# Kernel optimization log

Measured on AMD Instinct MI355X. Metric: run time of the kernel, lower is better.

Reference implementation:

```python
import jax, jax.numpy as jnp
import numpy as np
import math

N_FFT = 1024
HOP = 256
N_FRAMES = 16384
SR = 24000
FFT_BIN = N_FFT // 2 + 1
EPS = 1e-11


def hann(n):
    # torch.hann_window default (periodic=True)
    return 0.5 * (1.0 - jnp.cos(2.0 * jnp.pi * jnp.arange(n, dtype=jnp.float32) / n))


def linear_interp(x, scale):
    # x: [B, T] -> [B, T*scale]; matches F.interpolate(mode='linear', align_corners=False)
    T = x.shape[-1]
    pos = (jnp.arange(T * scale, dtype=jnp.float32) + 0.5) / scale - 0.5
    pos = jnp.clip(pos, 0.0, T - 1.0)
    lo = jnp.floor(pos).astype(jnp.int32)
    hi = jnp.minimum(lo + 1, T - 1)
    frac = pos - lo.astype(jnp.float32)
    return x[:, lo] * (1.0 - frac) + x[:, hi] * frac


def impulse_train(f0, hop_length, sample_rate):
    # f0: [B, n_frames] -> impulse train [B, n_frames*hop]
    f0_up = linear_interp(f0, hop_length)
    phase = jnp.cumsum(f0_up, axis=-1) / sample_rate
    saw = jnp.mod(phase, 1.0)
    imp = saw - jnp.roll(saw, -1, axis=-1) + f0_up / sample_rate
    # original runs under torch.no_grad()
    return jax.lax.stop_gradient(imp)


def stft(x, n_fft, hop, window):
    # torch.stft(center=True, pad_mode='reflect', onesided, normalized=False)
    pad = n_fft // 2
    xp = jnp.pad(x, ((0, 0), (pad, pad)), mode="reflect")
    nf = (xp.shape[-1] - n_fft) // hop + 1
    idx = jnp.arange(nf)[:, None] * hop + jnp.arange(n_fft)[None, :]
    frames = xp[:, idx] * window  # [B, nf, n_fft]
    return jnp.fft.rfft(frames, axis=-1).transpose(0, 2, 1)  # [B, bins, nf]


def istft(S, n_fft, hop, window):
    # torch.istft(center=True): windowed overlap-add, divide by sum of squared windows
    B = S.shape[0]
    frames = jnp.fft.irfft(S.transpose(0, 2, 1), n=n_fft, axis=-1) * window  # [B, nf, n_fft]
    nf = frames.shape[1]
    out_len = n_fft + (nf - 1) * hop
    idx = jnp.arange(nf)[:, None] * hop + jnp.arange(n_fft)[None, :]
    sig = jnp.zeros((B, out_len), frames.dtype).at[:, idx].add(frames)
    wsq = jnp.zeros((out_len,), frames.dtype).at[idx].add(
        jnp.broadcast_to(window * window, (nf, n_fft))
    )
    pad = n_fft // 2
    return sig[:, pad:-pad] / jnp.maximum(wsq[pad:-pad], EPS)


def spectral_envelope_filter(signal, envelope, n_fft, hop):
    w = hann(n_fft)
    S = stft(signal, n_fft, hop, w)[:, :, 1:]  # drop first frame -> [B, bins, n_frames]
    return istft(S * envelope, n_fft, hop, w)


def estimate_minimum_phase(amp):
    # amp: [B, bins, T] real positive envelope; cepstral min-phase along dim 1
    n = (amp.shape[1] - 1) * 2
    cep = jnp.fft.irfft(jnp.log(amp), n=n, axis=1)
    fold = jnp.concatenate(
        [jnp.ones((1,), jnp.float32),
         2.0 * jnp.ones((n // 2 - 1,), jnp.float32),
         jnp.ones((1,), jnp.float32),
         jnp.zeros((n // 2 - 1,), jnp.float32)]
    )
    cep = cep * fold[None, :, None]
    return jnp.exp(jnp.fft.rfft(cep, axis=1))  # complex min-phase spectrum [B, bins, T]


def setup_inputs() -> dict:
    key = jax.random.key(0)
    k1, k2, k3 = jax.random.split(key, 3)
    log_f0 = jnp.full((1, N_FRAMES), math.log(100.0), dtype=jnp.float32)
    spec_env_noi = jax.random.normal(k1, (1, FFT_BIN, N_FRAMES), jnp.float32) - 6.0
    spec_env_per = jax.random.normal(k2, (1, FFT_BIN, N_FRAMES), jnp.float32) - 6.0
    noise = jax.random.normal(k3, (1, HOP * N_FRAMES), jnp.float32)
    return {"log_f0": log_f0, "spec_env_noi": spec_env_noi,
            "spec_env_per": spec_env_per, "noise": noise}


def reference(log_f0, spec_env_noi, spec_env_per, noise):
    pulse = impulse_train(jnp.exp(log_f0), HOP, SR)
    noi = spectral_envelope_filter(noise, jnp.exp(spec_env_noi), N_FFT, HOP)
    per = spectral_envelope_filter(
        pulse, estimate_minimum_phase(jnp.exp(spec_env_per)), N_FFT, HOP
    )
    return noi + per  # [1, (N_FRAMES-1)*HOP]
```

## Files before the change

kernel.cpp:

```cpp
#include <hip/hip_runtime.h>
#include <math.h>

#define L_TOT 4194304
#define NFR   16384
#define OUTN  4194048


__device__ __forceinline__ int lvl_off(int a) {
  return L_TOT - (L_TOT >> (a - 1));
}

__device__ __forceinline__ int swz(int e) {
  return e ^ (((e >> 4) & 3) * 5);
}

__device__ __forceinline__ float f0_up_val(const float* f0arr, int j) {
  float pos = __fadd_rn(__fmul_rn(__fadd_rn((float)j, 0.5f), 1.0f / 256.0f), -0.5f);
  pos = fminf(fmaxf(pos, 0.0f), 16383.0f);
  int lo = (int)pos;
  int hi = min(lo + 1, NFR - 1);
  float frac = __fadd_rn(pos, -(float)lo);
  float a = __fmul_rn(f0arr[lo], __fadd_rn(1.0f, -frac));
  float b = __fmul_rn(f0arr[hi], frac);
  return __fadd_rn(a, b);
}

__device__ float prefix_sum(const float* W, const float* f0arr, int m) {
  float acc = 0.0f;
  bool first = true;
  int pos = 0;
  for (int a = 22; a >= 1; --a) {
    if (m & (1 << a)) {
      float node = W[lvl_off(a) + (pos >> a)];
      acc = first ? node : __fadd_rn(acc, node);
      first = false;
      pos += (1 << a);
    }
  }
  if (m & 1) {
    float node = f0_up_val(f0arr, pos);
    acc = first ? node : __fadd_rn(acc, node);
  }
  return acc;
}

__global__ __launch_bounds__(256) void init_tables(const float* __restrict__ logf0,
                                                   float* __restrict__ W) {
  int g = blockIdx.x * 256 + threadIdx.x;
  float* twc = W + 2 * L_TOT;
  float* tws = twc + 512;
  float* wh  = twc + 1024;
  float* f0arr = twc + 2048;
  if (g < 512) {
    double a = (double)g * 3.14159265358979323846 / 512.0;
    twc[g] = (float)cos(a);
    tws[g] = (float)sin(a);
  }
  if (g < 1024) {
    double a = (double)g * 3.14159265358979323846 / 512.0;
    wh[g] = (float)(0.5 - 0.5 * cos(a));
  }
  if (g >= 2048 && g < 2048 + NFR) {
    f0arr[g - 2048] = (float)exp((double)logf0[g - 2048]);
  }
}

__global__ __launch_bounds__(256) void tree_kernel(float* W) {
  const float* f0arr = W + 2 * L_TOT + 2048;
  __shared__ float A[2048];
  __shared__ float B[1024];
  int tid = threadIdx.x;
  int base = blockIdx.x * 2048;
  for (int i = tid; i < 2048; i += 256) A[i] = f0_up_val(f0arr, base + i);
  __syncthreads();
  float* src = A;
  float* dst = B;
  int cnt = 1024;
  for (int a = 1; a <= 11; ++a) {
    int gbase = base >> a;
    for (int i = tid; i < cnt; i += 256) {
      float v = __fadd_rn(src[2 * i], src[2 * i + 1]);
      dst[i] = v;
      if (a == 11) W[lvl_off(11) + gbase + i] = v;
    }
    __syncthreads();
    float* tmp = src; src = dst; dst = tmp;
    cnt >>= 1;
  }
}

__global__ __launch_bounds__(256) void tree_top_kernel(float* W) {
  __shared__ float A[2048];
  __shared__ float B[1024];
  int tid = threadIdx.x;
  for (int i = tid; i < 2048; i += 256) A[i] = W[lvl_off(11) + i];
  __syncthreads();
  float* src = A;
  float* dst = B;
  int cnt = 1024;
  for (int a = 12; a <= 22; ++a) {
    for (int i = tid; i < cnt; i += 256) {
      float v = __fadd_rn(src[2 * i], src[2 * i + 1]);
      dst[i] = v;
      W[lvl_off(a) + i] = v;
    }
    __syncthreads();
    float* tmp = src; src = dst; dst = tmp;
    cnt >>= 1;
  }
}

__global__ __launch_bounds__(256) void pulse_kernel(float* W) {
  const float* f0arr = W + 2 * L_TOT + 2048;
  __shared__ float Tl[510];
  __shared__ float P[4100];
  int tid = threadIdx.x;
  int base = blockIdx.x * 4096;

  float v[16];
#pragma unroll
  for (int c = 0; c < 16; ++c) v[c] = f0_up_val(f0arr, base + 16 * tid + c);
  float s2[8], s4[4], s8[2];
#pragma unroll
  for (int j = 0; j < 8; ++j) s2[j] = __fadd_rn(v[2 * j], v[2 * j + 1]);
#pragma unroll
  for (int j = 0; j < 4; ++j) s4[j] = __fadd_rn(s2[2 * j], s2[2 * j + 1]);
  s8[0] = __fadd_rn(s4[0], s4[1]);
  s8[1] = __fadd_rn(s4[2], s4[3]);
  Tl[tid] = __fadd_rn(s8[0], s8[1]);
  __syncthreads();
  if (tid < 128) Tl[256 + tid] = __fadd_rn(Tl[2 * tid], Tl[2 * tid + 1]);
  __syncthreads();
  if (tid < 64)  Tl[384 + tid] = __fadd_rn(Tl[256 + 2 * tid], Tl[256 + 2 * tid + 1]);
  __syncthreads();
  if (tid < 32)  Tl[448 + tid] = __fadd_rn(Tl[384 + 2 * tid], Tl[384 + 2 * tid + 1]);
  __syncthreads();
  if (tid < 16)  Tl[480 + tid] = __fadd_rn(Tl[448 + 2 * tid], Tl[448 + 2 * tid + 1]);
  __syncthreads();
  if (tid < 8)   Tl[496 + tid] = __fadd_rn(Tl[480 + 2 * tid], Tl[480 + 2 * tid + 1]);
  __syncthreads();
  if (tid < 4)   Tl[504 + tid] = __fadd_rn(Tl[496 + 2 * tid], Tl[496 + 2 * tid + 1]);
  __syncthreads();
  if (tid < 2)   Tl[508 + tid] = __fadd_rn(Tl[504 + 2 * tid], Tl[504 + 2 * tid + 1]);
  __syncthreads();

  float accT = 0.0f;
  bool firstT = true;
  {
    int pos = 0;
    for (int a = 22; a >= 12; --a) {
      if (base & (1 << a)) {
        float node = W[lvl_off(a) + (pos >> a)];
        accT = firstT ? node : __fadd_rn(accT, node);
        firstT = false;
        pos += (1 << a);
      }
    }
  }
  float accM = accT;
  bool firstM = firstT;
  {
    int rh = 16 * tid;
    int lpos = 0;
    for (int a = 11; a >= 4; --a) {
      if (rh & (1 << a)) {
        float node = Tl[512 - (512 >> (a - 4)) + (lpos >> a)];
        accM = firstM ? node : __fadd_rn(accM, node);
        firstM = false;
        lpos += (1 << a);
      }
    }
  }
  if (tid >= 1) P[16 * tid] = accM;
#pragma unroll
  for (int c = 1; c <= 15; ++c) {
    float acc = accM;
    bool first = firstM;
    int lp = 0;
    if (c & 8) { float n = s8[lp >> 3]; acc = first ? n : __fadd_rn(acc, n); first = false; lp += 8; }
    if (c & 4) { float n = s4[lp >> 2]; acc = first ? n : __fadd_rn(acc, n); first = false; lp += 4; }
    if (c & 2) { float n = s2[lp >> 1]; acc = first ? n : __fadd_rn(acc, n); first = false; lp += 2; }
    if (c & 1) { float n = v[lp];       acc = first ? n : __fadd_rn(acc, n); }
    P[16 * tid + c] = acc;
  }
  if (tid == 0) P[4096] = prefix_sum(W, f0arr, base + 4096);
  if (tid == 1) {
    int m2 = base + 4097;
    P[4097] = (m2 <= L_TOT) ? prefix_sum(W, f0arr, m2) : 0.0f;
  }
  __syncthreads();

  float o[16];
#pragma unroll
  for (int c = 0; c < 16; ++c) {
    int i = base + 16 * tid + c;
    float P1 = P[16 * tid + c + 1];
    float P2 = (i == L_TOT - 1) ? prefix_sum(W, f0arr, 1)
                                : P[16 * tid + c + 2];
    float t1 = __fdiv_rn(P1, 24000.0f);
    float saw1 = __fadd_rn(t1, -floorf(t1));
    float t2 = __fdiv_rn(P2, 24000.0f);
    float saw2 = __fadd_rn(t2, -floorf(t2));
    float cc = __fdiv_rn(v[c], 24000.0f);
    o[c] = __fadd_rn(__fadd_rn(saw1, -saw2), cc);
  }
#pragma unroll
  for (int k = 0; k < 4; ++k)
    *(float4*)&W[L_TOT + base + 16 * tid + 4 * k] =
        make_float4(o[4 * k], o[4 * k + 1], o[4 * k + 2], o[4 * k + 3]);
}

template <int DIR>
__device__ void fft1024_r4(float2* X, float2* Pb, const float2* tw) {
  int tid = threadIdx.x;
  float2* S = X;
  float2* D = Pb;
  __syncthreads();
#pragma unroll
  for (int s = 0; s < 5; ++s) {
    int m = 1 << (2 * s);
    int b = tid;
    int t = b & ~(m - 1);
    float2 twu = tw[t];
    float ur = twu.x, ui = (DIR > 0) ? twu.y : -twu.y;
    float vr = ur * ur - ui * ui;
    float vi = 2.0f * ur * ui;
    float w3r = ur * vr - ui * vi;
    float w3i = ur * vi + ui * vr;
    float2 x0 = S[swz(b)], x1 = S[swz(b + 256)], x2 = S[swz(b + 512)], x3 = S[swz(b + 768)];
    float s0r = x0.x + x2.x, s0i = x0.y + x2.y;
    float s1r = x1.x + x3.x, s1i = x1.y + x3.y;
    float d0r = x0.x - x2.x, d0i = x0.y - x2.y;
    float e1r = x1.x - x3.x, e1i = x1.y - x3.y;
    float ser = (DIR > 0) ? -e1i : e1i;
    float sei = (DIR > 0) ? e1r : -e1r;
    int d0 = b + 3 * t;
    D[swz(d0)] = make_float2(s0r + s1r, s0i + s1i);
    float t1r = d0r + ser, t1i = d0i + sei;
    D[swz(d0 + m)] = make_float2(t1r * ur - t1i * ui, t1r * ui + t1i * ur);
    float t2r = s0r - s1r, t2i = s0i - s1i;
    D[swz(d0 + 2 * m)] = make_float2(t2r * vr - t2i * vi, t2r * vi + t2i * vr);
    float t3r = d0r - ser, t3i = d0i - sei;
    D[swz(d0 + 3 * m)] = make_float2(t3r * w3r - t3i * w3i, t3r * w3i + t3i * w3r);
    __syncthreads();
    float2* tmp = S; S = D; D = tmp;
  }
}

__device__ __forceinline__ float hann_w(int i, const float2* tw) {
  int j = (i > 512) ? (1024 - i) : i;
  float c = (j <= 256) ? tw[j].x : -tw[512 - j].x;
  return 0.5f - 0.5f * c;
}

__device__ __forceinline__ void combine_one(int k, float An, const float2* Y, float2* H) {
  int k2 = (1024 - k) & 1023;
  float2 z = Y[swz(k)], mm = Y[swz(k2)];
  float Ar = 0.5f * (z.x + mm.x), Ai = 0.5f * (z.y - mm.y);
  float Br = 0.5f * (z.y + mm.y), Bi = 0.5f * (mm.x - z.x);
  float2 h = H[k];
  H[k] = make_float2(Br * h.x - Bi * h.y + Ar * An,
                     Br * h.y + Bi * h.x + Ai * An);
}

__global__ __launch_bounds__(256) void column_kernel(
    const float* __restrict__ noise,
    const float* __restrict__ envn,
    const float* __restrict__ envp,
    const float* __restrict__ W,
    float* __restrict__ out) {
  __shared__ float2 F[1024], Y[1024];
  __shared__ float2 hA[513], hB[513];
  __shared__ float2 tw[257];
  int tid = threadIdx.x;
  int bid = blockIdx.x;
  int g = (bid & 7) * 1024 + (bid >> 3);
  int fA = 2 * g;
  const float* pulse = W + L_TOT;
  const float* gtab = W + 2 * L_TOT;

  for (int i = tid; i < 257; i += 256) tw[i] = make_float2(gtab[i], gtab[512 + i]);
  for (int k = tid; k < 513; k += 256) {
    float2 e = *(const float2*)&envp[k * NFR + fA];
    hA[k] = e;
  }
  __syncthreads();

  for (int i = tid; i < 1024; i += 256) {
    int k = (i <= 512) ? i : 1024 - i;
    F[swz(i)] = hA[k];
  }
  fft1024_r4<+1>(F, Y, tw);
  {
    float2 a0 = Y[swz(tid)], a1 = Y[swz(tid + 256)], a2 = Y[swz(tid + 512)];
    float s0 = (tid == 0) ? (1.0f / 1024.0f) : (2.0f / 1024.0f);
    F[swz(tid)] = make_float2(a0.x * s0, a0.y * s0);
    F[swz(tid + 256)] = make_float2(a1.x * (2.0f / 1024.0f), a1.y * (2.0f / 1024.0f));
    F[swz(tid + 512)] = (tid == 0) ? make_float2(a2.x * (1.0f / 1024.0f),
                                                 a2.y * (1.0f / 1024.0f))
                                   : make_float2(0.0f, 0.0f);
    F[swz(tid + 768)] = make_float2(0.0f, 0.0f);
  }
  fft1024_r4<-1>(F, Y, tw);
  for (int k = tid; k < 513; k += 256) {
    int k2 = (1024 - k) & 1023;
    float2 z = Y[swz(k)], mm = Y[swz(k2)];
    float GAr = 0.5f * (z.x + mm.x), GAi = 0.5f * (z.y - mm.y);
    float GBr = 0.5f * (z.y + mm.y), GBi = 0.5f * (mm.x - z.x);
    float er = expf(GAr);
    float si, co;
    sincosf(GAi, &si, &co);
    hA[k] = make_float2(er * co, er * si);
    er = expf(GBr);
    sincosf(GBi, &si, &co);
    hB[k] = make_float2(er * co, er * si);
  }

  for (int i = tid; i < 1024; i += 256) {
    int q = 256 * fA - 256 + i;
    if (q < 0) q = -q;
    else if (q >= L_TOT) q = 2 * L_TOT - 2 - q;
    float wv = hann_w(i, tw);
    F[swz(i)] = make_float2(noise[q] * wv, pulse[q] * wv);
  }
  fft1024_r4<-1>(F, Y, tw);
  float2 eA0 = *(const float2*)&envn[tid * NFR + fA];
  combine_one(tid, expf(eA0.x), Y, hA);
  float2 eA1 = *(const float2*)&envn[(tid + 256) * NFR + fA];
  combine_one(tid + 256, expf(eA1.x), Y, hA);
  float2 eA2 = make_float2(0.0f, 0.0f);
  if (tid == 0) {
    eA2 = *(const float2*)&envn[512 * NFR + fA];
    combine_one(512, expf(eA2.x), Y, hA);
  }

  for (int i = tid; i < 1024; i += 256) {
    int q = 256 * fA + i;
    if (q >= L_TOT) q = 2 * L_TOT - 2 - q;
    float wv = hann_w(i, tw);
    F[swz(i)] = make_float2(noise[q] * wv, pulse[q] * wv);
  }
  fft1024_r4<-1>(F, Y, tw);
  combine_one(tid, expf(eA0.y), Y, hB);
  combine_one(tid + 256, expf(eA1.y), Y, hB);
  if (tid == 0) combine_one(512, expf(eA2.y), Y, hB);
  __syncthreads();

  for (int i = tid; i < 1024; i += 256) {
    if (i <= 512) {
      F[swz(i)] = make_float2(hA[i].x - hB[i].y, hA[i].y + hB[i].x);
    } else {
      int j = 1024 - i;
      F[swz(i)] = make_float2(hA[j].x + hB[j].y, hB[j].x - hA[j].y);
    }
  }
  fft1024_r4<+1>(F, Y, tw);
  const float sc = 1.0f / 1536.0f;
  for (int i = tid; i < 1280; i += 256) {
    float val = 0.0f;
    if (i < 1024) val = Y[swz(i)].x * (hann_w(i, tw) * sc);
    if (i >= 256) {
      int j = i - 256;
      val += Y[swz(j)].y * (hann_w(j, tw) * sc);
    }
    int t = 256 * fA - 512 + i;
    if (t >= 0 && t < OUTN) atomicAdd(&out[t], val);
  }
}

__global__ __launch_bounds__(256) void finalize_kernel(float* __restrict__ out,
                                                       const float* __restrict__ W) {
  const float* wh = W + 2 * L_TOT + 1024;
  int tid = threadIdx.x;
  int t = (blockIdx.x == 0) ? tid : (OUTN - 256 + tid);
  int p = t + 512;
  int jmin = max(0, (p - 768) >> 8);
  int jmax = min(NFR - 1, p >> 8);
  float wsq = 0.0f;
  for (int j = jmin; j <= jmax; ++j) {
    float w = wh[p - 256 * j];
    wsq += w * w;
  }
  out[t] = out[t] * (1.5f / fmaxf(wsq, 1e-11f));
}

extern "C" void kernel_launch(void* const* d_in, const int* in_sizes, int n_in,
                              void* d_out, int out_size, void* d_ws, size_t ws_size,
                              hipStream_t stream) {
  const float* logf0 = (const float*)d_in[0];
  const float* envn  = (const float*)d_in[1];
  const float* envp  = (const float*)d_in[2];
  const float* noise = (const float*)d_in[3];
  float* out = (float*)d_out;
  float* W = (float*)d_ws;

  init_tables<<<dim3(72), dim3(256), 0, stream>>>(logf0, W);
  tree_kernel<<<dim3(2048), dim3(256), 0, stream>>>(W);
  tree_top_kernel<<<dim3(1), dim3(256), 0, stream>>>(W);
  pulse_kernel<<<dim3(L_TOT / 4096), dim3(256), 0, stream>>>(W);
  hipMemsetAsync(d_out, 0, (size_t)out_size * sizeof(float), stream);
  column_kernel<<<dim3(NFR / 2), dim3(256), 0, stream>>>(noise, envn, envp, W, out);
  finalize_kernel<<<dim3(2), dim3(256), 0, stream>>>(out, W);
}
```

Measured before the change: 244.5 us.

## Use in-place DIF/DIT FFTs with digit-reversed ordering and register twiddles

Replaces the ping-pong Stockham radix-4 FFT with in-place DIF and DIT variants that share one LDS buffer, pairing them so the digit-reversed order between them cancels and spectral indexing goes through dr4. Twiddles and Hann window values are preloaded into registers instead of an LDS table, and the swizzle gains more XOR terms to reduce bank conflicts for the new access strides. Halving LDS use and adding launch_bounds(256,8) targets higher occupancy, at the cost of extra syncs and a more complex index mapping.

Result: slower. 675.8 us (+176.4%).

```diff
diff --git a/kernel.cpp b/kernel.cpp
--- a/kernel.cpp
+++ b/kernel.cpp
@@ -11,7 +11,13 @@
 }
 
 __device__ __forceinline__ int swz(int e) {
-  return e ^ (((e >> 4) & 3) * 5);
+  int h = (e >> 4) & 3, g = (e >> 6) & 3, f = (e >> 8) & 3;
+  return e ^ (h * 5) ^ (g * 3) ^ ((f * 12) & 15);
+}
+
+__device__ __forceinline__ int dr4(int p) {
+  return ((p & 3) << 8) | (((p >> 2) & 3) << 6) | (((p >> 4) & 3) << 4) |
+         (((p >> 6) & 3) << 2) | ((p >> 8) & 3);
 }
 
 __device__ __forceinline__ float f0_up_val(const float* f0arr, int j) {
@@ -211,51 +217,74 @@
 }
 
 template <int DIR>
-__device__ void fft1024_r4(float2* X, float2* Pb, const float2* tw) {
-  int tid = threadIdx.x;
-  float2* S = X;
-  float2* D = Pb;
+__device__ __forceinline__ void fft_dif(float2* F, const float2 (&twr)[4]) {
+  int tid = threadIdx.x;
   __syncthreads();
 #pragma unroll
   for (int s = 0; s < 5; ++s) {
-    int m = 1 << (2 * s);
-    int b = tid;
-    int t = b & ~(m - 1);
-    float2 twu = tw[t];
-    float ur = twu.x, ui = (DIR > 0) ? twu.y : -twu.y;
-    float vr = ur * ur - ui * ui;
-    float vi = 2.0f * ur * ui;
-    float w3r = ur * vr - ui * vi;
-    float w3i = ur * vi + ui * vr;
-    float2 x0 = S[swz(b)], x1 = S[swz(b + 256)], x2 = S[swz(b + 512)], x3 = S[swz(b + 768)];
+    int L = 256 >> (2 * s);
+    int q = tid & (L - 1);
+    int base = ((tid >> (8 - 2 * s)) << (10 - 2 * s)) | q;
+    float ur, ui;
+    if (s < 4) { ur = twr[s].x; ui = twr[s].y; } else { ur = 1.0f; ui = 0.0f; }
+    if (DIR < 0) ui = -ui;
+    int e0 = swz(base), e1 = swz(base + L), e2 = swz(base + 2 * L), e3 = swz(base + 3 * L);
+    float2 x0 = F[e0], x1 = F[e1], x2 = F[e2], x3 = F[e3];
     float s0r = x0.x + x2.x, s0i = x0.y + x2.y;
     float s1r = x1.x + x3.x, s1i = x1.y + x3.y;
     float d0r = x0.x - x2.x, d0i = x0.y - x2.y;
-    float e1r = x1.x - x3.x, e1i = x1.y - x3.y;
-    float ser = (DIR > 0) ? -e1i : e1i;
-    float sei = (DIR > 0) ? e1r : -e1r;
-    int d0 = b + 3 * t;
-    D[swz(d0)] = make_float2(s0r + s1r, s0i + s1i);
-    float t1r = d0r + ser, t1i = d0i + sei;
-    D[swz(d0 + m)] = make_float2(t1r * ur - t1i * ui, t1r * ui + t1i * ur);
-    float t2r = s0r - s1r, t2i = s0i - s1i;
-    D[swz(d0 + 2 * m)] = make_float2(t2r * vr - t2i * vi, t2r * vi + t2i * vr);
-    float t3r = d0r - ser, t3i = d0i - sei;
-    D[swz(d0 + 3 * m)] = make_float2(t3r * w3r - t3i * w3i, t3r * w3i + t3i * w3r);
+    float ddr = x1.x - x3.x, ddi = x1.y - x3.y;
+    float t3r = (DIR > 0) ? -ddi : ddi;
+    float t3i = (DIR > 0) ? ddr : -ddr;
+    float vr = ur * ur - ui * ui, vi = 2.0f * ur * ui;
+    float w3r = ur * vr - ui * vi, w3i = ur * vi + ui * vr;
+    F[e0] = make_float2(s0r + s1r, s0i + s1i);
+    float a1r = d0r + t3r, a1i = d0i + t3i;
+    F[e1] = make_float2(a1r * ur - a1i * ui, a1r * ui + a1i * ur);
+    float a2r = s0r - s1r, a2i = s0i - s1i;
+    F[e2] = make_float2(a2r * vr - a2i * vi, a2r * vi + a2i * vr);
+    float a3r = d0r - t3r, a3i = d0i - t3i;
+    F[e3] = make_float2(a3r * w3r - a3i * w3i, a3r * w3i + a3i * w3r);
     __syncthreads();
-    float2* tmp = S; S = D; D = tmp;
-  }
-}
-
-__device__ __forceinline__ float hann_w(int i, const float2* tw) {
-  int j = (i > 512) ? (1024 - i) : i;
-  float c = (j <= 256) ? tw[j].x : -tw[512 - j].x;
-  return 0.5f - 0.5f * c;
-}
-
-__device__ __forceinline__ void combine_one(int k, float An, const float2* Y, float2* H) {
+  }
+}
+
+template <int DIR>
+__device__ __forceinline__ void fft_dit(float2* F, const float2 (&twr)[4]) {
+  int tid = threadIdx.x;
+  __syncthreads();
+#pragma unroll
+  for (int s = 0; s < 5; ++s) {
+    int L = 1 << (2 * s);
+    int q = tid & (L - 1);
+    int base = ((tid >> (2 * s)) << (2 * s + 2)) | q;
+    float ur, ui;
+    if (s > 0) { ur = twr[4 - s].x; ui = twr[4 - s].y; } else { ur = 1.0f; ui = 0.0f; }
+    if (DIR < 0) ui = -ui;
+    int e0 = swz(base), e1 = swz(base + L), e2 = swz(base + 2 * L), e3 = swz(base + 3 * L);
+    float2 x0 = F[e0], x1 = F[e1], x2 = F[e2], x3 = F[e3];
+    float vr = ur * ur - ui * ui, vi = 2.0f * ur * ui;
+    float w3r = ur * vr - ui * vi, w3i = ur * vi + ui * vr;
+    float b1r = x1.x * ur - x1.y * ui, b1i = x1.x * ui + x1.y * ur;
+    float b2r = x2.x * vr - x2.y * vi, b2i = x2.x * vi + x2.y * vr;
+    float b3r = x3.x * w3r - x3.y * w3i, b3i = x3.x * w3i + x3.y * w3r;
+    float s0r = x0.x + b2r, s0i = x0.y + b2i;
+    float d0r = x0.x - b2r, d0i = x0.y - b2i;
+    float s1r = b1r + b3r, s1i = b1i + b3i;
+    float ddr = b1r - b3r, ddi = b1i - b3i;
+    float d1r = (DIR > 0) ? -ddi : ddi;
+    float d1i = (DIR > 0) ? ddr : -ddr;
+    F[e0] = make_float2(s0r + s1r, s0i + s1i);
+    F[e1] = make_float2(d0r + d1r, d0i + d1i);
+    F[e2] = make_float2(s0r - s1r, s0i - s1i);
+    F[e3] = make_float2(d0r - d1r, d0i - d1i);
+    __syncthreads();
+  }
+}
+
+__device__ __forceinline__ void combine_one(int k, float An, const float2* F, float2* H) {
   int k2 = (1024 - k) & 1023;
-  float2 z = Y[swz(k)], mm = Y[swz(k2)];
+  float2 z = F[swz(dr4(k))], mm = F[swz(dr4(k2))];
   float Ar = 0.5f * (z.x + mm.x), Ai = 0.5f * (z.y - mm.y);
   float Br = 0.5f * (z.y + mm.y), Bi = 0.5f * (mm.x - z.x);
   float2 h = H[k];
@@ -263,48 +292,61 @@
                      Br * h.y + Bi * h.x + Ai * An);
 }
 
-__global__ __launch_bounds__(256) void column_kernel(
+__global__ __launch_bounds__(256, 8) void column_kernel(
     const float* __restrict__ noise,
     const float* __restrict__ envn,
     const float* __restrict__ envp,
     const float* __restrict__ W,
     float* __restrict__ out) {
-  __shared__ float2 F[1024], Y[1024];
+  __shared__ float2 F[1024];
   __shared__ float2 hA[513], hB[513];
-  __shared__ float2 tw[257];
   int tid = threadIdx.x;
   int bid = blockIdx.x;
   int g = (bid & 7) * 1024 + (bid >> 3);
   int fA = 2 * g;
   const float* pulse = W + L_TOT;
   const float* gtab = W + 2 * L_TOT;
-
-  for (int i = tid; i < 257; i += 256) tw[i] = make_float2(gtab[i], gtab[512 + i]);
+  const float* whg = gtab + 1024;
+
+  float2 twr[4];
+  {
+    int x1 = (tid & 63) << 2, x2 = (tid & 15) << 4, x3 = (tid & 3) << 6;
+    twr[0] = make_float2(gtab[tid], gtab[512 + tid]);
+    twr[1] = make_float2(gtab[x1], gtab[512 + x1]);
+    twr[2] = make_float2(gtab[x2], gtab[512 + x2]);
+    twr[3] = make_float2(gtab[x3], gtab[512 + x3]);
+  }
+  float wvr[4];
+#pragma unroll
+  for (int k = 0; k < 4; ++k) wvr[k] = whg[tid + 256 * k];
+
   for (int k = tid; k < 513; k += 256) {
     float2 e = *(const float2*)&envp[k * NFR + fA];
     hA[k] = e;
   }
   __syncthreads();
 
-  for (int i = tid; i < 1024; i += 256) {
+#pragma unroll
+  for (int j = 0; j < 4; ++j) {
+    int i = tid + 256 * j;
     int k = (i <= 512) ? i : 1024 - i;
     F[swz(i)] = hA[k];
   }
-  fft1024_r4<+1>(F, Y, tw);
-  {
-    float2 a0 = Y[swz(tid)], a1 = Y[swz(tid + 256)], a2 = Y[swz(tid + 512)];
-    float s0 = (tid == 0) ? (1.0f / 1024.0f) : (2.0f / 1024.0f);
-    F[swz(tid)] = make_float2(a0.x * s0, a0.y * s0);
-    F[swz(tid + 256)] = make_float2(a1.x * (2.0f / 1024.0f), a1.y * (2.0f / 1024.0f));
-    F[swz(tid + 512)] = (tid == 0) ? make_float2(a2.x * (1.0f / 1024.0f),
-                                                 a2.y * (1.0f / 1024.0f))
-                                   : make_float2(0.0f, 0.0f);
-    F[swz(tid + 768)] = make_float2(0.0f, 0.0f);
-  }
-  fft1024_r4<-1>(F, Y, tw);
+  fft_dif<+1>(F, twr);
+#pragma unroll
+  for (int j = 0; j < 4; ++j) {
+    int p = tid + 256 * j;
+    int k = dr4(p);
+    float sc = ((k & 511) == 0) ? (1.0f / 1024.0f)
+                                : ((k < 512) ? (2.0f / 1024.0f) : 0.0f);
+    int e = swz(p);
+    float2 a = F[e];
+    F[e] = make_float2(a.x * sc, a.y * sc);
+  }
+  fft_dit<-1>(F, twr);
   for (int k = tid; k < 513; k += 256) {
     int k2 = (1024 - k) & 1023;
-    float2 z = Y[swz(k)], mm = Y[swz(k2)];
+    float2 z = F[swz(k)], mm = F[swz(k2)];
     float GAr = 0.5f * (z.x + mm.x), GAi = 0.5f * (z.y - mm.y);
     float GBr = 0.5f * (z.y + mm.y), GBi = 0.5f * (mm.x - z.x);
     float er = expf(GAr);
@@ -315,54 +357,63 @@
     sincosf(GBi, &si, &co);
     hB[k] = make_float2(er * co, er * si);
   }
-
-  for (int i = tid; i < 1024; i += 256) {
+  __syncthreads();
+
+#pragma unroll
+  for (int j = 0; j < 4; ++j) {
+    int i = tid + 256 * j;
     int q = 256 * fA - 256 + i;
     if (q < 0) q = -q;
     else if (q >= L_TOT) q = 2 * L_TOT - 2 - q;
-    float wv = hann_w(i, tw);
+    float wv = wvr[j];
     F[swz(i)] = make_float2(noise[q] * wv, pulse[q] * wv);
   }
-  fft1024_r4<-1>(F, Y, tw);
+  fft_dif<-1>(F, twr);
   float2 eA0 = *(const float2*)&envn[tid * NFR + fA];
-  combine_one(tid, expf(eA0.x), Y, hA);
+  combine_one(tid, expf(eA0.x), F, hA);
   float2 eA1 = *(const float2*)&envn[(tid + 256) * NFR + fA];
-  combine_one(tid + 256, expf(eA1.x), Y, hA);
+  combine_one(tid + 256, expf(eA1.x), F, hA);
   float2 eA2 = make_float2(0.0f, 0.0f);
   if (tid == 0) {
     eA2 = *(const float2*)&envn[512 * NFR + fA];
-    combine_one(512, expf(eA2.x), Y, hA);
-  }
-
-  for (int i = tid; i < 1024; i += 256) {
+    combine_one(512, expf(eA2.x), F, hA);
+  }
+  __syncthreads();
+
+#pragma unroll
+  for (int j = 0; j < 4; ++j) {
+    int i = tid + 256 * j;
     int q = 256 * fA + i;
     if (q >= L_TOT) q = 2 * L_TOT - 2 - q;
-    float wv = hann_w(i, tw);
+    float wv = wvr[j];
     F[swz(i)] = make_float2(noise[q] * wv, pulse[q] * wv);
   }
-  fft1024_r4<-1>(F, Y, tw);
-  combine_one(tid, expf(eA0.y), Y, hB);
-  combine_one(tid + 256, expf(eA1.y), Y, hB);
-  if (tid == 0) combine_one(512, expf(eA2.y), Y, hB);
-  __syncthreads();
-
-  for (int i = tid; i < 1024; i += 256) {
+  fft_dif<-1>(F, twr);
+  combine_one(tid, expf(eA0.y), F, hB);
+  combine_one(tid + 256, expf(eA1.y), F, hB);
+  if (tid == 0) combine_one(512, expf(eA2.y), F, hB);
+  __syncthreads();
+
+#pragma unroll
+  for (int j = 0; j < 4; ++j) {
+    int i = tid + 256 * j;
+    float2 zv;
     if (i <= 512) {
-      F[swz(i)] = make_float2(hA[i].x - hB[i].y, hA[i].y + hB[i].x);
+      zv = make_float2(hA[i].x - hB[i].y, hA[i].y + hB[i].x);
     } else {
-      int j = 1024 - i;
-      F[swz(i)] = make_float2(hA[j].x + hB[j].y, hB[j].x - hA[j].y);
-    }
-  }
-  fft1024_r4<+1>(F, Y, tw);
-  const float sc = 1.0f / 1536.0f;
-  for (int i = tid; i < 1280; i += 256) {
+      int jj = 1024 - i;
+      zv = make_float2(hA[jj].x + hB[jj].y, hB[jj].x - hA[jj].y);
+    }
+    F[swz(dr4(i))] = zv;
+  }
+  fft_dit<+1>(F, twr);
+  const float scl = 1.0f / 1536.0f;
+#pragma unroll
+  for (int j = 0; j < 5; ++j) {
+    int i = tid + 256 * j;
     float val = 0.0f;
-    if (i < 1024) val = Y[swz(i)].x * (hann_w(i, tw) * sc);
-    if (i >= 256) {
-      int j = i - 256;
-      val += Y[swz(j)].y * (hann_w(j, tw) * sc);
-    }
+    if (j < 4) val = F[swz(i)].x * (wvr[j] * scl);
+    if (j > 0) val += F[swz(i - 256)].y * (wvr[j - 1] * scl);
     int t = 256 * fA - 512 + i;
     if (t >= 0 && t < OUTN) atomicAdd(&out[t], val);
   }
```
